# Kernel optimization log

Hardware: AMD Instinct MI355X
Metric: run time of the kernel (lower is better)

Reference implementation:

```python
import jax, jax.numpy as jnp
import numpy as np

B, T, D1, D2, DM, V, K = 2, 512, 256, 128, 1024, 32000, 4
SCALE = 0.05  # keep tanh/sigmoid out of full saturation with randn params


def setup_inputs() -> dict:
    key = jax.random.key(0)
    ks = jax.random.split(key, 7)
    s = lambda k, shape: SCALE * jax.random.normal(k, shape, dtype=jnp.float32)
    return {
        "gc": jax.random.normal(ks[0], (B, T, D1), dtype=jnp.float32),
        "H": s(ks[1], (K, DM, D1)),
        "U": s(ks[2], (K, D2, D1)),
        "v": s(ks[3], (V, D2)),
        "u": s(ks[4], (K, D1)),
        "b": s(ks[5], (V, K)),
        "emb": s(ks[6], (V, DM)),
    }


def reference(gc, H, U, v, u, b, emb):
    # gc: (B,T,D1)
    hc = jnp.tanh(jnp.einsum('kdi,bti->btkd', H, gc))        # (B,T,K,DM)
    tU = jnp.tanh(jnp.einsum('kji,bti->btkj', U, gc))        # (B,T,K,D2)
    # token- and context-dependent gate logits: (B,T,V,K)
    lc = (jnp.einsum('vj,btkj->btvk', v, tU)
          + jnp.einsum('ki,bti->btk', u, gc)[:, :, None, :]
          + b[None, None])
    gamma = jax.nn.sigmoid(lc[..., :K - 1])                  # (B,T,V,3)
    g0, g1, g2 = gamma[..., 0], gamma[..., 1], gamma[..., 2]
    # sigmoid-tree mixture priors: (B,T,V,K)
    pi = jnp.stack([g0 * g1, g0 * (1.0 - g1),
                    (1.0 - g0) * g2, (1.0 - g0) * (1.0 - g2)], axis=-1)
    # contract hc with embeddings per gate FIRST (avoids btikj blow-up),
    # then weight by pi -- same math as the original pi (x) emb outer product.
    dots = jnp.einsum('btkd,vd->btvk', hc, emb)              # (B,T,V,K)
    logits = jnp.sum(pi * dots, axis=-1)                     # (B,T,V)
    return jax.nn.softmax(logits, axis=-1)
```

## Files before the change

### kernel.cpp

```cpp
#include <hip/hip_runtime.h>
#include <math.h>

namespace {

typedef _Float16 f16;
typedef _Float16 f16x8 __attribute__((ext_vector_type(8)));
typedef float    f32x4 __attribute__((ext_vector_type(4)));

constexpr int kBT = 1024, kD1 = 256, kD2 = 128, kDM = 1024, kV = 32000, kK = 4;
constexpr int AR = kBT * kK;
constexpr int ROWS_H = kK * kDM;
constexpr int ROWS_U = kK * kD2;
constexpr int ROWS_ALL = ROWS_H + ROWS_U + kK;
constexpr int SLICES = 8;
constexpr int SLICE_ROWS = (ROWS_ALL + SLICES - 1) / SLICES;
constexpr int NBY = kV / 128;

constexpr int PREP_BLOCKS = (kBT / 8) * SLICES;
constexpr int CVTV_BLOCKS = (kV * kD2 / 8) / 256;
constexpr int CVTE_BLOCKS = (kV * kDM / 8) / 256;

__global__ __launch_bounds__(256) void prep_cvt(
    const float* __restrict__ gc, const float* __restrict__ Hm,
    const float* __restrict__ Um, const float* __restrict__ um,
    const float* __restrict__ vmat, const float* __restrict__ emb,
    f16* __restrict__ hc, f16* __restrict__ tu, float* __restrict__ ug,
    f16* __restrict__ v16, f16* __restrict__ e16)
{
    __shared__ float sgc[8][kD1];
    const int bid = blockIdx.x;

    if (bid >= PREP_BLOCKS) {
        const float* src;
        f16* dst;
        int i;
        if (bid < PREP_BLOCKS + CVTV_BLOCKS) {
            src = vmat; dst = v16;
            i = (bid - PREP_BLOCKS) * 256 + threadIdx.x;
        } else {
            src = emb; dst = e16;
            i = (bid - PREP_BLOCKS - CVTV_BLOCKS) * 256 + threadIdx.x;
        }
        const float4 x0 = *reinterpret_cast<const float4*>(src + (size_t)i * 8);
        const float4 x1 = *reinterpret_cast<const float4*>(src + (size_t)i * 8 + 4);
        union { f16 h[8]; uint4 v; } u;
        u.h[0] = (f16)x0.x; u.h[1] = (f16)x0.y; u.h[2] = (f16)x0.z; u.h[3] = (f16)x0.w;
        u.h[4] = (f16)x1.x; u.h[5] = (f16)x1.y; u.h[6] = (f16)x1.z; u.h[7] = (f16)x1.w;
        *reinterpret_cast<uint4*>(dst + (size_t)i * 8) = u.v;
        return;
    }

    const int pbx = bid & 127;
    const int pby = bid >> 7;
    const int btBase = pbx * 8;
    for (int idx = threadIdx.x; idx < 8 * kD1; idx += 256)
        sgc[idx / kD1][idx % kD1] = gc[(size_t)btBase * kD1 + idx];
    __syncthreads();

    const int rStart = pby * SLICE_ROWS;
    int rEnd = rStart + SLICE_ROWS;
    if (rEnd > ROWS_ALL) rEnd = ROWS_ALL;
    for (int r = rStart + (int)threadIdx.x; r < rEnd; r += 256) {
        const float* wrow;
        if (r < ROWS_H)               wrow = Hm + (size_t)r * kD1;
        else if (r < ROWS_H + ROWS_U) wrow = Um + (size_t)(r - ROWS_H) * kD1;
        else                          wrow = um + (size_t)(r - ROWS_H - ROWS_U) * kD1;

        float acc[8] = {0.f,0.f,0.f,0.f,0.f,0.f,0.f,0.f};
        for (int i = 0; i < kD1; i += 4) {
            const float4 w = *reinterpret_cast<const float4*>(wrow + i);
            #pragma unroll
            for (int b = 0; b < 8; ++b) {
                const float4 g = *reinterpret_cast<const float4*>(&sgc[b][i]);
                acc[b] = fmaf(w.x, g.x, acc[b]);
                acc[b] = fmaf(w.y, g.y, acc[b]);
                acc[b] = fmaf(w.z, g.z, acc[b]);
                acc[b] = fmaf(w.w, g.w, acc[b]);
            }
        }
        #pragma unroll
        for (int b = 0; b < 8; ++b) {
            const int bt = btBase + b;
            if (r < ROWS_H) {
                const int k = r >> 10, d = r & 1023;
                hc[((size_t)(bt * kK + k) << 10) + d] = (f16)tanhf(acc[b]);
            } else if (r < ROWS_H + ROWS_U) {
                const int r2 = r - ROWS_H;
                const int k = r2 >> 7, j = r2 & 127;
                tu[(size_t)(bt * kK + k) * kD2 + j] = (f16)tanhf(acc[b]);
            } else {
                ug[bt * kK + (r - ROWS_H - ROWS_U)] = acc[b];
            }
        }
    }
}

__device__ __forceinline__ uint packf16x2(float a, float b) {
    union { f16 h[2]; uint u; } z;
    z.h[0] = (f16)a; z.h[1] = (f16)b;
    return z.u;
}

__global__ __launch_bounds__(256, 2) void fused_mfma(
    const f16* __restrict__ hc,  const f16* __restrict__ tu,
    const f16* __restrict__ v16, const f16* __restrict__ e16,
    const float* __restrict__ ug, const float* __restrict__ bmat,
    f16* __restrict__ lg16, float* __restrict__ psum)
{
    __shared__ __align__(16) f16 sA[2][128 * 64];
    __shared__ __align__(16) f16 sB[2][128 * 64];

    const int tid  = threadIdx.x;
    const int lane = tid & 63;
    const int wave = tid >> 6;
    const int fr = lane & 15, fq = lane >> 4;
    const int wrow = wave >> 1, wcol = wave & 1;
    const int aRowBase = blockIdx.x * 128;
    const int vBase    = blockIdx.y * 128;
    const int btB      = blockIdx.x * 32 + wrow * 16;

    const int srow = lane >> 3;
    const int scol = ((lane & 7) ^ srow) * 8;

    const f16* gApt = tu  + (size_t)(aRowBase + wave * 32 + srow) * kD2 + scol;
    const f16* gBpt = v16 + (size_t)(vBase    + wave * 32 + srow) * kD2 + scol;
    const f16* sApt = hc  + (size_t)(aRowBase + wave * 32 + srow) * kDM + scol;
    const f16* sBpt = e16 + (size_t)(vBase    + wave * 32 + srow) * kDM + scol;

    f16* dA = &sA[0][0] + wave * 4 * 512;
    f16* dB = &sB[0][0] + wave * 4 * 512;

#define GLD(SRC, DST)                                                         \
    __builtin_amdgcn_global_load_lds(                                         \
        (const __attribute__((address_space(1))) void*)(SRC),                 \
        (__attribute__((address_space(3))) void*)(DST), 16, 0, 0)

    auto stage_gate = [&](int t) {
        #pragma unroll
        for (int i = 0; i < 4; ++i) {
            GLD(gApt + t * 64 + i * 8 * kD2, dA + t * 8192 + i * 512);
            GLD(gBpt + t * 64 + i * 8 * kD2, dB + t * 8192 + i * 512);
        }
    };
    auto stage_dots = [&](int buf) {
        #pragma unroll
        for (int i = 0; i < 4; ++i) {
            GLD(sApt + i * 8 * kDM, dA + buf * 8192 + i * 512);
            GLD(sBpt + i * 8 * kDM, dB + buf * 8192 + i * 512);
        }
        sApt += 64; sBpt += 64;
    };

    const int ps0 = (fq ^ (fr & 7)) * 8;
    const int ps1 = ((4 + fq) ^ (fr & 7)) * 8;
    const f16* rA0 = &sA[0][0] + (wrow * 64 + fr) * 64 + ps0;
    const f16* rA1 = &sA[0][0] + (wrow * 64 + fr) * 64 + ps1;
    const f16* rB0 = &sB[0][0] + (wcol * 64 + fr) * 64 + ps0;
    const f16* rB1 = &sB[0][0] + (wcol * 64 + fr) * 64 + ps1;

    auto mmStep = [&](f32x4 (&acc)[4][4], int q) {
        const int qo = q * 8192;
        {
            f16x8 a[4], b[4];
            #pragma unroll
            for (int m = 0; m < 4; ++m)
                a[m] = *reinterpret_cast<const f16x8*>(rA0 + qo + m * 1024);
            #pragma unroll
            for (int n = 0; n < 4; ++n)
                b[n] = *reinterpret_cast<const f16x8*>(rB0 + qo + n * 1024);
            __builtin_amdgcn_s_setprio(1);
            #pragma unroll
            for (int m = 0; m < 4; ++m)
                #pragma unroll
                for (int n = 0; n < 4; ++n)
                    acc[m][n] = __builtin_amdgcn_mfma_f32_16x16x32_f16(
                        a[m], b[n], acc[m][n], 0, 0, 0);
            __builtin_amdgcn_s_setprio(0);
        }
        {
            f16x8 a[4], b[4];
            #pragma unroll
            for (int m = 0; m < 4; ++m)
                a[m] = *reinterpret_cast<const f16x8*>(rA1 + qo + m * 1024);
            #pragma unroll
            for (int n = 0; n < 4; ++n)
                b[n] = *reinterpret_cast<const f16x8*>(rB1 + qo + n * 1024);
            __builtin_amdgcn_s_setprio(1);
            #pragma unroll
            for (int m = 0; m < 4; ++m)
                #pragma unroll
                for (int n = 0; n < 4; ++n)
                    acc[m][n] = __builtin_amdgcn_mfma_f32_16x16x32_f16(
                        a[m], b[n], acc[m][n], 0, 0, 0);
            __builtin_amdgcn_s_setprio(0);
        }
    };

#define WAITBAR(VM)                                                           \
    asm volatile("s_waitcnt vmcnt(" VM ")" ::: "memory");                     \
    __builtin_amdgcn_s_barrier();                                             \
    asm volatile("" ::: "memory");
#define ENDBAR                                                                \
    asm volatile("" ::: "memory");                                            \
    __builtin_amdgcn_s_barrier();                                             \
    asm volatile("" ::: "memory");

    const f32x4 zz = {0.f, 0.f, 0.f, 0.f};

    f32x4 gacc[4][4];
    #pragma unroll
    for (int m = 0; m < 4; ++m)
        #pragma unroll
        for (int n = 0; n < 4; ++n) gacc[m][n] = zz;

    stage_gate(0);
    stage_gate(1);          WAITBAR("8")  mmStep(gacc, 0);  ENDBAR
    stage_dots(0);          WAITBAR("8")  mmStep(gacc, 1);  ENDBAR

    uint pi01[4][4], pi23[4][4];
    {
        float4 bb[4];
        #pragma unroll
        for (int n = 0; n < 4; ++n)
            bb[n] = *reinterpret_cast<const float4*>(
                bmat + (size_t)(vBase + wcol * 64 + n * 16 + fr) * 4);
        #pragma unroll
        for (int m = 0; m < 4; ++m) {
            const float4 ugv = *reinterpret_cast<const float4*>(
                ug + (btB + m * 4 + fq) * 4);
            #pragma unroll
            for (int n = 0; n < 4; ++n) {
                const float l0 = gacc[m][n][0] + ugv.x + bb[n].x;
                const float l1 = gacc[m][n][1] + ugv.y + bb[n].y;
                const float l2 = gacc[m][n][2] + ugv.z + bb[n].z;
                const float g0 = 1.f / (1.f + __expf(-l0));
                const float g1 = 1.f / (1.f + __expf(-l1));
                const float g2 = 1.f / (1.f + __expf(-l2));
                pi01[m][n] = packf16x2(g0 * g1, g0 * (1.f - g1));
                pi23[m][n] = packf16x2((1.f - g0) * g2, (1.f - g0) * (1.f - g2));
            }
        }
    }

    f32x4 dacc[4][4];
    #pragma unroll
    for (int m = 0; m < 4; ++m)
        #pragma unroll
        for (int n = 0; n < 4; ++n) dacc[m][n] = zz;

    for (int it = 0; it < 7; ++it) {
        stage_dots(1);      WAITBAR("8")  mmStep(dacc, 0);  ENDBAR
        stage_dots(0);      WAITBAR("8")  mmStep(dacc, 1);  ENDBAR
    }
    stage_dots(1);          WAITBAR("8")  mmStep(dacc, 0);  ENDBAR
                            WAITBAR("0")  mmStep(dacc, 1);
#undef WAITBAR
#undef ENDBAR
#undef GLD

    #pragma unroll
    for (int m = 0; m < 4; ++m) {
        const int bt = btB + m * 4 + fq;
        float es = 0.f;
        #pragma unroll
        for (int n = 0; n < 4; ++n) {
            const int v = vBase + wcol * 64 + n * 16 + fr;
            union { uint u; f16 h[2]; } p01, p23;
            p01.u = pi01[m][n]; p23.u = pi23[m][n];
            const float lg = (float)p01.h[0] * dacc[m][n][0]
                           + (float)p01.h[1] * dacc[m][n][1]
                           + (float)p23.h[0] * dacc[m][n][2]
                           + (float)p23.h[1] * dacc[m][n][3];
            const f16 lh = (f16)lg;
            lg16[(size_t)bt * kV + v] = lh;
            es += __expf((float)lh);
        }
        es += __shfl_xor(es, 1);
        es += __shfl_xor(es, 2);
        es += __shfl_xor(es, 4);
        es += __shfl_xor(es, 8);
        if (fr == 0)
            psum[(size_t)bt * 512 + blockIdx.y * 2 + wcol] = es;
    }
}

__global__ __launch_bounds__(256) void softmax_kernel(
    float* __restrict__ out, const f16* __restrict__ lg16,
    const float* __restrict__ psum)
{
    __shared__ float red[4];
    const int bt = blockIdx.x;
    const f16* row16 = lg16 + (size_t)bt * kV;
    float* row = out + (size_t)bt * kV;
    const int tid = threadIdx.x;

    float s = 0.f;
    for (int i = tid; i < 2 * NBY; i += 256) s += psum[(size_t)bt * 512 + i];
    #pragma unroll
    for (int o = 1; o < 64; o <<= 1) s += __shfl_xor(s, o);
    if ((tid & 63) == 0) red[tid >> 6] = s;
    __syncthreads();
    s = red[0] + red[1] + red[2] + red[3];
    const float inv = 1.f / s;

    for (int i = tid * 8; i < kV; i += 2048) {
        union { uint4 v; f16 h[8]; } u;
        u.v = *reinterpret_cast<const uint4*>(row16 + i);
        float4 y0, y1;
        y0.x = __expf((float)u.h[0]) * inv;
        y0.y = __expf((float)u.h[1]) * inv;
        y0.z = __expf((float)u.h[2]) * inv;
        y0.w = __expf((float)u.h[3]) * inv;
        y1.x = __expf((float)u.h[4]) * inv;
        y1.y = __expf((float)u.h[5]) * inv;
        y1.z = __expf((float)u.h[6]) * inv;
        y1.w = __expf((float)u.h[7]) * inv;
        *reinterpret_cast<float4*>(row + i)     = y0;
        *reinterpret_cast<float4*>(row + i + 4) = y1;
    }
}

}

extern "C" void kernel_launch(void* const* d_in, const int* in_sizes, int n_in,
                              void* d_out, int out_size, void* d_ws, size_t ws_size,
                              hipStream_t stream)
{
    (void)in_sizes; (void)n_in; (void)out_size; (void)ws_size;
    const float* gc   = (const float*)d_in[0];
    const float* Hm   = (const float*)d_in[1];
    const float* Um   = (const float*)d_in[2];
    const float* vmat = (const float*)d_in[3];
    const float* um   = (const float*)d_in[4];
    const float* bmat = (const float*)d_in[5];
    const float* emb  = (const float*)d_in[6];
    float* out = (float*)d_out;

    size_t off = 0;
    auto take = [&](size_t bytes) -> char* {
        char* p = (char*)d_ws + off;
        off += (bytes + 255) & ~(size_t)255;
        return p;
    };
    f16*   hc   = (f16*)  take((size_t)AR * kDM * 2);
    f16*   tu   = (f16*)  take((size_t)AR * kD2 * 2);
    f16*   v16  = (f16*)  take((size_t)kV * kD2 * 2);
    f16*   e16  = (f16*)  take((size_t)kV * kDM * 2);
    float* ug   = (float*)take((size_t)AR * 4);
    float* psum = (float*)take((size_t)kBT * 512 * 4);
    f16*   lg16 = (f16*)  take((size_t)kBT * kV * 2);

    prep_cvt<<<dim3(PREP_BLOCKS + CVTV_BLOCKS + CVTE_BLOCKS), 256, 0, stream>>>(
        gc, Hm, Um, um, vmat, emb, hc, tu, ug, v16, e16);
    fused_mfma<<<dim3(AR / 128, NBY), 256, 0, stream>>>(
        hc, tu, v16, e16, ug, bmat, lg16, psum);
    softmax_kernel<<<dim3(kBT), 256, 0, stream>>>(out, lg16, psum);
}
```

Baseline: 517.8 us.

## Split fused gate/dots kernel into separate gate and larger-tile dots GEMMs

The fused MFMA kernel is split in two. A gate kernel computes the tU·v gate logits, applies the sigmoid tree and stores the four mixture weights per (bt,v) as packed f16 in a new workspace buffer. A dots kernel then runs the hc·emb GEMM with 256x256 tiles, 512 threads and a 4-stage global-to-LDS pipeline, and weights the result by the stored priors. This aims to raise MFMA efficiency and operand reuse in the dominant GEMM. The cost is writing and re-reading a roughly 256 MB prior buffer, and the new path only runs when the workspace is large enough.

```diff
diff --git a/kernel.cpp b/kernel.cpp
--- a/kernel.cpp
+++ b/kernel.cpp
@@ -101,6 +101,258 @@
     return z.u;
 }
 
+__global__ __launch_bounds__(256, 2) void gate_mfma(
+    const f16* __restrict__ tu, const f16* __restrict__ v16,
+    const float* __restrict__ ug, const float* __restrict__ bmat,
+    uint2* __restrict__ piBuf)
+{
+    __shared__ __align__(16) f16 sA[2][128 * 64];
+    __shared__ __align__(16) f16 sB[2][128 * 64];
+
+    const int tid  = threadIdx.x;
+    const int lane = tid & 63;
+    const int wave = tid >> 6;
+    const int fr = lane & 15, fq = lane >> 4;
+    const int wrow = wave >> 1, wcol = wave & 1;
+    const int aRowBase = blockIdx.x * 128;
+    const int vBase    = blockIdx.y * 128;
+    const int btB      = blockIdx.x * 32 + wrow * 16;
+
+    const int srow = lane >> 3;
+    const int scol = ((lane & 7) ^ srow) * 8;
+
+    const f16* gApt = tu  + (size_t)(aRowBase + wave * 32 + srow) * kD2 + scol;
+    const f16* gBpt = v16 + (size_t)(vBase    + wave * 32 + srow) * kD2 + scol;
+    f16* dA = &sA[0][0] + wave * 4 * 512;
+    f16* dB = &sB[0][0] + wave * 4 * 512;
+
+#define GLD(SRC, DST)                                                         \
+    __builtin_amdgcn_global_load_lds(                                         \
+        (const __attribute__((address_space(1))) void*)(SRC),                 \
+        (__attribute__((address_space(3))) void*)(DST), 16, 0, 0)
+
+    auto stage_gate = [&](int t) {
+        #pragma unroll
+        for (int i = 0; i < 4; ++i) {
+            GLD(gApt + t * 64 + i * 8 * kD2, dA + t * 8192 + i * 512);
+            GLD(gBpt + t * 64 + i * 8 * kD2, dB + t * 8192 + i * 512);
+        }
+    };
+
+    const int ps0 = (fq ^ (fr & 7)) * 8;
+    const int ps1 = ((4 + fq) ^ (fr & 7)) * 8;
+    const f16* rA0 = &sA[0][0] + (wrow * 64 + fr) * 64 + ps0;
+    const f16* rA1 = &sA[0][0] + (wrow * 64 + fr) * 64 + ps1;
+    const f16* rB0 = &sB[0][0] + (wcol * 64 + fr) * 64 + ps0;
+    const f16* rB1 = &sB[0][0] + (wcol * 64 + fr) * 64 + ps1;
+
+    auto mmStep = [&](f32x4 (&acc)[4][4], int q) {
+        const int qo = q * 8192;
+        {
+            f16x8 a[4], b[4];
+            #pragma unroll
+            for (int m = 0; m < 4; ++m)
+                a[m] = *reinterpret_cast<const f16x8*>(rA0 + qo + m * 1024);
+            #pragma unroll
+            for (int n = 0; n < 4; ++n)
+                b[n] = *reinterpret_cast<const f16x8*>(rB0 + qo + n * 1024);
+            #pragma unroll
+            for (int m = 0; m < 4; ++m)
+                #pragma unroll
+                for (int n = 0; n < 4; ++n)
+                    acc[m][n] = __builtin_amdgcn_mfma_f32_16x16x32_f16(
+                        a[m], b[n], acc[m][n], 0, 0, 0);
+        }
+        {
+            f16x8 a[4], b[4];
+            #pragma unroll
+            for (int m = 0; m < 4; ++m)
+                a[m] = *reinterpret_cast<const f16x8*>(rA1 + qo + m * 1024);
+            #pragma unroll
+            for (int n = 0; n < 4; ++n)
+                b[n] = *reinterpret_cast<const f16x8*>(rB1 + qo + n * 1024);
+            #pragma unroll
+            for (int m = 0; m < 4; ++m)
+                #pragma unroll
+                for (int n = 0; n < 4; ++n)
+                    acc[m][n] = __builtin_amdgcn_mfma_f32_16x16x32_f16(
+                        a[m], b[n], acc[m][n], 0, 0, 0);
+        }
+    };
+
+    f32x4 gacc[4][4];
+    const f32x4 zz = {0.f, 0.f, 0.f, 0.f};
+    #pragma unroll
+    for (int m = 0; m < 4; ++m)
+        #pragma unroll
+        for (int n = 0; n < 4; ++n) gacc[m][n] = zz;
+
+    stage_gate(0);
+    stage_gate(1);
+    asm volatile("s_waitcnt vmcnt(8)" ::: "memory");
+    __builtin_amdgcn_s_barrier();
+    asm volatile("" ::: "memory");
+    mmStep(gacc, 0);
+    asm volatile("" ::: "memory");
+    __builtin_amdgcn_s_barrier();
+    asm volatile("s_waitcnt vmcnt(0)" ::: "memory");
+    __builtin_amdgcn_s_barrier();
+    asm volatile("" ::: "memory");
+    mmStep(gacc, 1);
+#undef GLD
+
+    float4 bb[4];
+    #pragma unroll
+    for (int n = 0; n < 4; ++n)
+        bb[n] = *reinterpret_cast<const float4*>(
+            bmat + (size_t)(vBase + wcol * 64 + n * 16 + fr) * 4);
+    #pragma unroll
+    for (int m = 0; m < 4; ++m) {
+        const int bt = btB + m * 4 + fq;
+        const float4 ugv = *reinterpret_cast<const float4*>(ug + bt * 4);
+        #pragma unroll
+        for (int n = 0; n < 4; ++n) {
+            const int v = vBase + wcol * 64 + n * 16 + fr;
+            const float l0 = gacc[m][n][0] + ugv.x + bb[n].x;
+            const float l1 = gacc[m][n][1] + ugv.y + bb[n].y;
+            const float l2 = gacc[m][n][2] + ugv.z + bb[n].z;
+            const float g0 = 1.f / (1.f + __expf(-l0));
+            const float g1 = 1.f / (1.f + __expf(-l1));
+            const float g2 = 1.f / (1.f + __expf(-l2));
+            uint2 pv;
+            pv.x = packf16x2(g0 * g1, g0 * (1.f - g1));
+            pv.y = packf16x2((1.f - g0) * g2, (1.f - g0) * (1.f - g2));
+            piBuf[(size_t)bt * kV + v] = pv;
+        }
+    }
+}
+
+__global__ __launch_bounds__(512, 2) void dots_mfma(
+    const f16* __restrict__ hc, const f16* __restrict__ e16,
+    const uint2* __restrict__ piBuf,
+    f16* __restrict__ lg16, float* __restrict__ psum)
+{
+    __shared__ __align__(16) f16 sA[4][256 * 32];
+    __shared__ __align__(16) f16 sB[4][256 * 32];
+
+    const int tid  = threadIdx.x;
+    const int lane = tid & 63;
+    const int wave = tid >> 6;
+    const int fr = lane & 15, fq = lane >> 4;
+    const int wm = wave >> 2, wc = wave & 3;
+
+    const int bx = blockIdx.x;
+    const int by = blockIdx.y;
+    const int aRowBase = bx * 256;
+    const int vBase    = by * 256;
+    const int btB      = bx * 64 + wm * 32;
+
+    const int srowL = lane >> 2;
+    const int scolL = ((lane & 3) ^ ((lane >> 3) & 3)) * 8;
+
+    const f16* pA = hc  + (size_t)(aRowBase + srowL) * kDM + scolL;
+    const f16* pB = e16 + (size_t)(vBase    + srowL) * kDM + scolL;
+
+    f16* dA0 = &sA[0][0] + (wave * 2 + 0) * 512;
+    f16* dA1 = &sA[0][0] + (wave * 2 + 1) * 512;
+    f16* dB0 = &sB[0][0] + (wave * 2 + 0) * 512;
+    f16* dB1 = &sB[0][0] + (wave * 2 + 1) * 512;
+
+    const int rslot = (fq ^ ((fr >> 1) & 3)) * 8;
+    const f16* rA = &sA[0][0] + (wm * 128 + fr) * 32 + rslot;
+    const f16* rB = &sB[0][0] + (wc * 64  + fr) * 32 + rslot;
+
+#define GLD(SRC, DST)                                                         \
+    __builtin_amdgcn_global_load_lds(                                         \
+        (const __attribute__((address_space(1))) void*)(SRC),                 \
+        (__attribute__((address_space(3))) void*)(DST), 16, 0, 0)
+
+#define STG(G) do {                                                           \
+        constexpr int SL_  = (G) & 3;                                         \
+        constexpr int COL_ = (G) * 32;                                        \
+        constexpr int CS_  = kDM * 16;                                        \
+        GLD(pA + COL_ + (wave * 2 + 0) * CS_, dA0 + SL_ * 8192);              \
+        GLD(pA + COL_ + (wave * 2 + 1) * CS_, dA1 + SL_ * 8192);              \
+        GLD(pB + COL_ + (wave * 2 + 0) * CS_, dB0 + SL_ * 8192);              \
+        GLD(pB + COL_ + (wave * 2 + 1) * CS_, dB1 + SL_ * 8192);              \
+    } while (0)
+
+#define PHASE(G, VM, DOSTG)                                                   \
+    {                                                                         \
+        DOSTG;                                                                \
+        asm volatile("s_waitcnt vmcnt(" VM ")" ::: "memory");                 \
+        __builtin_amdgcn_s_barrier();                                         \
+        asm volatile("" ::: "memory");                                        \
+        constexpr int SL_ = (G) & 3;                                          \
+        f16x8 bfr_[4];                                                        \
+        _Pragma("unroll")                                                     \
+        for (int n = 0; n < 4; ++n)                                           \
+            bfr_[n] = *reinterpret_cast<const f16x8*>(                        \
+                rB + SL_ * 8192 + n * 512);                                   \
+        __builtin_amdgcn_s_setprio(1);                                        \
+        _Pragma("unroll")                                                     \
+        for (int m = 0; m < 8; ++m) {                                         \
+            const f16x8 afr_ = *reinterpret_cast<const f16x8*>(               \
+                rA + SL_ * 8192 + m * 512);                                   \
+            _Pragma("unroll")                                                 \
+            for (int n = 0; n < 4; ++n)                                       \
+                acc[m][n] = __builtin_amdgcn_mfma_f32_16x16x32_f16(           \
+                    afr_, bfr_[n], acc[m][n], 0, 0, 0);                       \
+        }                                                                     \
+        __builtin_amdgcn_s_setprio(0);                                        \
+        asm volatile("" ::: "memory");                                        \
+        __builtin_amdgcn_s_barrier();                                         \
+        asm volatile("" ::: "memory");                                        \
+    }
+#define PH(G) PHASE(G, "8", STG((G) + 3))
+#define PH4(G) PH(G) PH((G) + 1) PH((G) + 2) PH((G) + 3)
+
+    f32x4 acc[8][4];
+    const f32x4 zz = {0.f, 0.f, 0.f, 0.f};
+    #pragma unroll
+    for (int m = 0; m < 8; ++m)
+        #pragma unroll
+        for (int n = 0; n < 4; ++n) acc[m][n] = zz;
+
+    STG(0); STG(1); STG(2);
+    PH4(0) PH4(4) PH4(8) PH4(12) PH4(16) PH4(20) PH4(24)
+    PH(28)
+    PHASE(29, "4", (void)0)
+    PHASE(30, "0", (void)0)
+    PHASE(31, "0", (void)0)
+#undef PH4
+#undef PH
+#undef PHASE
+#undef STG
+#undef GLD
+
+    #pragma unroll
+    for (int m = 0; m < 8; ++m) {
+        const int bt = btB + m * 4 + fq;
+        float es = 0.f;
+        #pragma unroll
+        for (int n = 0; n < 4; ++n) {
+            const int v = vBase + wc * 64 + n * 16 + fr;
+            const uint2 pv = piBuf[(size_t)bt * kV + v];
+            union { uint u; f16 h[2]; } p01, p23;
+            p01.u = pv.x; p23.u = pv.y;
+            const float lg = (float)p01.h[0] * acc[m][n][0]
+                           + (float)p01.h[1] * acc[m][n][1]
+                           + (float)p23.h[0] * acc[m][n][2]
+                           + (float)p23.h[1] * acc[m][n][3];
+            const f16 lh = (f16)lg;
+            lg16[(size_t)bt * kV + v] = lh;
+            es += __expf((float)lh);
+        }
+        es += __shfl_xor(es, 1);
+        es += __shfl_xor(es, 2);
+        es += __shfl_xor(es, 4);
+        es += __shfl_xor(es, 8);
+        if (fr == 0)
+            psum[(size_t)bt * 512 + by * 4 + wc] = es;
+    }
+}
+
 __global__ __launch_bounds__(256, 2) void fused_mfma(
     const f16* __restrict__ hc,  const f16* __restrict__ tu,
     const f16* __restrict__ v16, const f16* __restrict__ e16,
@@ -295,7 +547,7 @@
     const int tid = threadIdx.x;
 
     float s = 0.f;
-    for (int i = tid; i < 2 * NBY; i += 256) s += psum[(size_t)bt * 512 + i];
+    for (int i = tid; i < 500; i += 256) s += psum[(size_t)bt * 512 + i];
     #pragma unroll
     for (int o = 1; o < 64; o <<= 1) s += __shfl_xor(s, o);
     if ((tid & 63) == 0) red[tid >> 6] = s;
@@ -326,7 +578,7 @@
                               void* d_out, int out_size, void* d_ws, size_t ws_size,
                               hipStream_t stream)
 {
-    (void)in_sizes; (void)n_in; (void)out_size; (void)ws_size;
+    (void)in_sizes; (void)n_in; (void)out_size;
     const float* gc   = (const float*)d_in[0];
     const float* Hm   = (const float*)d_in[1];
     const float* Um   = (const float*)d_in[2];
@@ -349,10 +601,19 @@
     float* ug   = (float*)take((size_t)AR * 4);
     float* psum = (float*)take((size_t)kBT * 512 * 4);
     f16*   lg16 = (f16*)  take((size_t)kBT * kV * 2);
+    uint2* piBuf = (uint2*)take((size_t)kBT * kV * 8);
+    const bool split = (ws_size >= off);
 
     prep_cvt<<<dim3(PREP_BLOCKS + CVTV_BLOCKS + CVTE_BLOCKS), 256, 0, stream>>>(
         gc, Hm, Um, um, vmat, emb, hc, tu, ug, v16, e16);
-    fused_mfma<<<dim3(AR / 128, NBY), 256, 0, stream>>>(
-        hc, tu, v16, e16, ug, bmat, lg16, psum);
+    if (split) {
+        gate_mfma<<<dim3(AR / 128, NBY), 256, 0, stream>>>(
+            tu, v16, ug, bmat, piBuf);
+        dots_mfma<<<dim3(AR / 256, kV / 256), 512, 0, stream>>>(
+            hc, e16, piBuf, lg16, psum);
+    } else {
+        fused_mfma<<<dim3(AR / 128, NBY), 256, 0, stream>>>(
+            hc, tu, v16, e16, ug, bmat, lg16, psum);
+    }
     softmax_kernel<<<dim3(kBT), 256, 0, stream>>>(out, lg16, psum);
 }
```

Result: slower. 635.9 us (+22.8%).
